# Kernel optimization log

Measured on AMD Instinct MI355X. Metric: run time of the kernel, lower is better.

Reference implementation:

```python
import jax, jax.numpy as jnp
import numpy as np

D_MODEL = 1024
N_HEADS = 16
HEAD_DIM = D_MODEL // N_HEADS
D_FF = 4096
LN_EPS = 1e-5


def setup_inputs() -> dict:
    key = jax.random.key(0)
    ks = jax.random.split(key, 13)
    s = lambda fan_in: 1.0 / np.sqrt(fan_in)
    return {
        "x": jax.random.normal(ks[0], (2, 2048, D_MODEL), dtype=jnp.float32),
        "w_qkv": jax.random.uniform(ks[1], (D_MODEL, 3 * D_MODEL), jnp.float32, -s(D_MODEL), s(D_MODEL)),
        "b_qkv": jax.random.uniform(ks[2], (3 * D_MODEL,), jnp.float32, -s(D_MODEL), s(D_MODEL)),
        "w_out": jax.random.uniform(ks[3], (D_MODEL, D_MODEL), jnp.float32, -s(D_MODEL), s(D_MODEL)),
        "b_out": jax.random.uniform(ks[4], (D_MODEL,), jnp.float32, -s(D_MODEL), s(D_MODEL)),
        "w_ff1": jax.random.uniform(ks[5], (D_MODEL, D_FF), jnp.float32, -s(D_MODEL), s(D_MODEL)),
        "b_ff1": jax.random.uniform(ks[6], (D_FF,), jnp.float32, -s(D_MODEL), s(D_MODEL)),
        "w_ff2": jax.random.uniform(ks[7], (D_FF, D_MODEL), jnp.float32, -s(D_FF), s(D_FF)),
        "b_ff2": jax.random.uniform(ks[8], (D_MODEL,), jnp.float32, -s(D_FF), s(D_FF)),
        "ln1_g": jnp.ones((D_MODEL,), jnp.float32),
        "ln1_b": jnp.zeros((D_MODEL,), jnp.float32),
        "ln2_g": jnp.ones((D_MODEL,), jnp.float32),
        "ln2_b": jnp.zeros((D_MODEL,), jnp.float32),
    }


def _layer_norm(x, g, b):
    mu = jnp.mean(x, axis=-1, keepdims=True)
    var = jnp.mean(jnp.square(x - mu), axis=-1, keepdims=True)
    return (x - mu) * jax.lax.rsqrt(var + LN_EPS) * g + b


def reference(x, w_qkv, b_qkv, w_out, b_out, w_ff1, b_ff1, w_ff2, b_ff2,
              ln1_g, ln1_b, ln2_g, ln2_b):
    B, S, D = x.shape
    scale = HEAD_DIM ** -0.5
    qkv = x @ w_qkv + b_qkv                                   # [B,S,3D]
    qkv = qkv.reshape(B, S, 3, N_HEADS, HEAD_DIM)
    q, k, v = (qkv[:, :, 0], qkv[:, :, 1], qkv[:, :, 2])      # [B,S,H,Dh]
    attn = jnp.einsum("bqhd,bkhd->bhqk", q, k) * scale        # [B,H,S,S]
    attn = jax.nn.softmax(attn, axis=-1)
    o = jnp.einsum("bhqk,bkhd->bqhd", attn, v).reshape(B, S, D)
    o = o @ w_out + b_out
    x = _layer_norm(x + o, ln1_g, ln1_b)
    # FFN: Linear -> exact GELU -> Linear (dropout = 0)
    h = jax.nn.gelu(x @ w_ff1 + b_ff1, approximate=False)
    ff = h @ w_ff2 + b_ff2
    x = _layer_norm(x + ff, ln2_g, ln2_b)
    return x
```

## Files before the change

kernel.cpp:

```cpp
#include <hip/hip_runtime.h>
#include <hip/hip_bf16.h>
#include <cstdint>
#include <cstddef>

using bf16 = __hip_bfloat16;
typedef __attribute__((ext_vector_type(8))) short bf16x8;
typedef __attribute__((ext_vector_type(4))) float f32x4;

#define TOKENS 4096
#define DMODEL 1024
#define DFF    4096
#define SEQ    2048
#define NHEAD  16
#define HDIM   64
#define KVBLK  64
#define NT     (SEQ / KVBLK)
#define QSCALE 0.1803368801111f

__device__ __forceinline__ void async16(const void* g, void* l) {
  __builtin_amdgcn_global_load_lds(
      (const __attribute__((address_space(1))) void*)g,
      (__attribute__((address_space(3))) void*)l, 16, 0, 0);
}

__device__ __forceinline__ f32x4 mfma16(bf16x8 a, bf16x8 b, f32x4 c) {
  return __builtin_amdgcn_mfma_f32_16x16x32_bf16(a, b, c, 0, 0, 0);
}

__device__ __forceinline__ float exp2_fast(float x) {
  float r;
  asm("v_exp_f32 %0, %1" : "=v"(r) : "v"(x));
  return r;
}

__device__ __forceinline__ float gelu_fast(float x) {
  const float z = fabsf(x) * 0.70710678118f;
  const float t = __builtin_amdgcn_rcpf(1.f + 0.3275911f * z);
  float p = 1.061405429f;
  p = p * t - 1.453152027f;
  p = p * t + 1.421413741f;
  p = p * t - 0.284496736f;
  p = p * t + 0.254829592f;
  const float e = exp2_fast(-z * z * 1.44269504089f);
  float erf = 1.f - p * t * e;
  erf = (x < 0.f) ? -erf : erf;
  return 0.5f * x * (1.f + erf);
}

__global__ void cast_bf16_k(const float* __restrict__ src, bf16* __restrict__ dst, int n) {
  int i = (blockIdx.x * blockDim.x + threadIdx.x) * 4;
  if (i >= n) return;
  float4 v = *(const float4*)(src + i);
  dst[i + 0] = __float2bfloat16(v.x);
  dst[i + 1] = __float2bfloat16(v.y);
  dst[i + 2] = __float2bfloat16(v.z);
  dst[i + 3] = __float2bfloat16(v.w);
}

__global__ void transpose_cast_k(const float* __restrict__ src, bf16* __restrict__ dst,
                                 int K, int N) {
  __shared__ float tile[32][33];
  int nt = blockIdx.x * 32, kt = blockIdx.y * 32;
  int tx = threadIdx.x, ty = threadIdx.y;
  #pragma unroll
  for (int i = 0; i < 32; i += 8)
    tile[ty + i][tx] = src[(size_t)(kt + ty + i) * N + nt + tx];
  __syncthreads();
  #pragma unroll
  for (int i = 0; i < 32; i += 8)
    dst[(size_t)(nt + ty + i) * K + kt + tx] = __float2bfloat16(tile[tx][ty + i]);
}

template <int EPI, int BN>
__global__ __launch_bounds__(256, 2)
void gemm_bt(const bf16* __restrict__ A, const bf16* __restrict__ Bt,
             const float* __restrict__ bias, int M, int N, int K,
             float* __restrict__ outf, bf16* __restrict__ outb,
             const float* __restrict__ resid,
             bf16* __restrict__ Qb, bf16* __restrict__ Kb, bf16* __restrict__ Vtb) {
  constexpr int MR = (BN == 128) ? 4 : 2;
  __shared__ bf16 Al[2][128 * 32];
  __shared__ bf16 Bl[2][BN * 32];
  const int t = threadIdx.x;
  const int nwg = gridDim.x * gridDim.y;
  const int flat = blockIdx.y * gridDim.x + blockIdx.x;
  const int swz = (flat & 7) * (nwg >> 3) + (flat >> 3);
  const int bm = (swz / gridDim.x) * 128, bn = (swz % gridDim.x) * BN;
  const int wid = t >> 6, lane = t & 63, g = lane >> 4, r = lane & 15;
  const int wr = (BN == 128) ? (wid >> 1) * 64 : wid * 32;
  const int wc = (BN == 128) ? (wid & 1) * 64 : 0;

  const f32x4 zero = {0.f, 0.f, 0.f, 0.f};
  f32x4 acc[MR][4];
  #pragma unroll
  for (int i = 0; i < MR; i++)
    #pragma unroll
    for (int j = 0; j < 4; j++) acc[i][j] = zero;

  const int ar0 = t >> 2, ac = (t & 3) * 8;
  const int ar1 = ar0 + 64;
  const int ach0 = t * 16, ach1 = ach0 + 4096;

  const int NK = K >> 5;
  #define STAGE(ktile, pb)                                                          \
    do {                                                                            \
      const int kk = (ktile) << 5;                                                  \
      async16(A + (size_t)(bm + ar0) * K + kk + ac, (char*)Al[pb] + ach0);          \
      async16(A + (size_t)(bm + ar1) * K + kk + ac, (char*)Al[pb] + ach1);          \
      async16(Bt + (size_t)(bn + ar0) * K + kk + ac, (char*)Bl[pb] + ach0);         \
      if constexpr (BN == 128)                                                      \
        async16(Bt + (size_t)(bn + ar1) * K + kk + ac, (char*)Bl[pb] + ach1);       \
    } while (0)

  STAGE(0, 0);
  asm volatile("s_waitcnt vmcnt(0)" ::: "memory");
  __builtin_amdgcn_s_barrier();

  #pragma unroll 1
  for (int it = 0; it < NK; ++it) {
    const int cur = it & 1;
    if (it + 1 < NK) STAGE(it + 1, cur ^ 1);
    bf16x8 af[MR], bfr[4];
    #pragma unroll
    for (int mt = 0; mt < MR; mt++)
      af[mt] = *(const bf16x8*)&Al[cur][(wr + mt * 16 + r) * 32 + 8 * g];
    #pragma unroll
    for (int nt = 0; nt < 4; nt++)
      bfr[nt] = *(const bf16x8*)&Bl[cur][(wc + nt * 16 + r) * 32 + 8 * g];
    #pragma unroll
    for (int mt = 0; mt < MR; mt++)
      #pragma unroll
      for (int nt = 0; nt < 4; nt++)
        acc[mt][nt] = mfma16(af[mt], bfr[nt], acc[mt][nt]);
    __builtin_amdgcn_sched_barrier(0);
    asm volatile("s_waitcnt vmcnt(0)" ::: "memory");
    __builtin_amdgcn_s_barrier();
  }
  #undef STAGE

  #pragma unroll
  for (int nt = 0; nt < 4; nt++) {
    const int col = bn + wc + nt * 16 + r;
    const float bv = bias[col];
    #pragma unroll
    for (int mt = 0; mt < MR; mt++) {
      #pragma unroll
      for (int j = 0; j < 4; j++) {
        const int row = bm + wr + mt * 16 + 4 * g + j;
        float v = acc[mt][nt][j] + bv;
        if constexpr (EPI == 0) {
          const int part = col >> 10, hd = col & 1023, h = hd >> 6, d = hd & 63;
          const int b_ = row >> 11, s_ = row & 2047;
          if (part == 0) {
            Qb[((size_t)(b_ * NHEAD + h) * SEQ + s_) * HDIM + d] =
                __float2bfloat16(v * QSCALE);
          } else if (part == 1) {
            Kb[((size_t)(b_ * NHEAD + h) * SEQ + s_) * HDIM + d] = __float2bfloat16(v);
          } else {
            Vtb[((size_t)(b_ * NHEAD + h) * HDIM + d) * SEQ + s_] = __float2bfloat16(v);
          }
        } else if constexpr (EPI == 1) {
          const size_t idx = (size_t)row * N + col;
          outf[idx] = v + resid[idx];
        } else {
          const size_t idx = (size_t)row * N + col;
          outb[idx] = __float2bfloat16(gelu_fast(v));
        }
      }
    }
  }
}

__global__ __launch_bounds__(256, 4)
void attn_k(const bf16* __restrict__ Q, const bf16* __restrict__ Km,
            const bf16* __restrict__ Vt, bf16* __restrict__ O) {
  __shared__ bf16 Kl[2][KVBLK * 64];
  __shared__ bf16 Vl[2][KVBLK * 64];
  __shared__ bf16 P[4][16 * 64];
  const int b = blockIdx.x;
  const int bswz = (b & 7) * 128 + (b >> 3);
  const int bh = bswz >> 5, qb = bswz & 31;
  const int t = threadIdx.x, wid = t >> 6, lane = t & 63, g = lane >> 4, r = lane & 15;
  const int q0 = qb * 64 + wid * 16;
  const bf16* Qp = Q + (size_t)bh * SEQ * HDIM;
  const char* Kc = (const char*)(Km + (size_t)bh * SEQ * HDIM);
  const char* Vc = (const char*)(Vt + (size_t)bh * HDIM * SEQ);

  const bf16x8 qf0 = *(const bf16x8*)&Qp[(q0 + r) * HDIM + 8 * g];
  const bf16x8 qf1 = *(const bf16x8*)&Qp[(q0 + r) * HDIM + 8 * g + 32];

  const int o0 = wid * 2048 + lane * 16, o1 = o0 + 1024;
  const int cs0 = ((((o0 >> 4) & 7) ^ ((o0 >> 7) & 7)) << 4);
  const int cs1 = ((((o1 >> 4) & 7) ^ ((o1 >> 7) & 7)) << 4);
  const int kso0 = (o0 & ~127) + cs0, kso1 = (o1 & ~127) + cs1;
  const int vso0 = (o0 >> 7) * (SEQ * 2) + cs0, vso1 = (o1 >> 7) * (SEQ * 2) + cs1;

  const f32x4 zero = {0.f, 0.f, 0.f, 0.f};
  f32x4 oacc[4];
  #pragma unroll
  for (int i = 0; i < 4; i++) oacc[i] = zero;
  float mrow = -1e30f, lrow = 0.f;
  bf16* pl = P[wid];
  const int cA = ((g ^ (r & 7)) << 3), cB = (((g + 4) ^ (r & 7)) << 3);

  {
    char* kd = (char*)Kl[0]; char* vd = (char*)Vl[0];
    async16(Kc + kso0, kd + o0); async16(Kc + kso1, kd + o1);
    async16(Vc + vso0, vd + o0); async16(Vc + vso1, vd + o1);
  }

  #pragma unroll 1
  for (int tt = 0; tt < NT; ++tt) {
    if (tt + 1 < NT) {
      const char* ks = Kc + (tt + 1) * (KVBLK * HDIM * 2);
      const char* vs = Vc + (tt + 1) * (KVBLK * 2);
      char* kd = (char*)Kl[(tt + 1) & 1]; char* vd = (char*)Vl[(tt + 1) & 1];
      async16(ks + kso0, kd + o0); async16(ks + kso1, kd + o1);
      async16(vs + vso0, vd + o0); async16(vs + vso1, vd + o1);
      asm volatile("s_waitcnt vmcnt(4)" ::: "memory");
    } else {
      asm volatile("s_waitcnt vmcnt(0)" ::: "memory");
    }
    __builtin_amdgcn_sched_barrier(0);
    __builtin_amdgcn_s_barrier();
    __builtin_amdgcn_sched_barrier(0);

    const bf16* kbuf = Kl[tt & 1];
    const bf16* vbuf = Vl[tt & 1];

    f32x4 sacc[4];
    #pragma unroll
    for (int kt = 0; kt < 4; kt++) {
      const bf16* krow = kbuf + (kt * 16 + r) * 64;
      bf16x8 ka = *(const bf16x8*)&krow[cA];
      bf16x8 kb = *(const bf16x8*)&krow[cB];
      f32x4 s = zero;
      s = mfma16(ka, qf0, s);
      s = mfma16(kb, qf1, s);
      sacc[kt] = s;
    }

    float m0 = fmaxf(fmaxf(sacc[0][0], sacc[0][1]), fmaxf(sacc[0][2], sacc[0][3]));
    float m1 = fmaxf(fmaxf(sacc[1][0], sacc[1][1]), fmaxf(sacc[1][2], sacc[1][3]));
    float m2 = fmaxf(fmaxf(sacc[2][0], sacc[2][1]), fmaxf(sacc[2][2], sacc[2][3]));
    float m3 = fmaxf(fmaxf(sacc[3][0], sacc[3][1]), fmaxf(sacc[3][2], sacc[3][3]));
    float mx = fmaxf(fmaxf(m0, m1), fmaxf(m2, m3));
    mx = fmaxf(mx, __shfl_xor(mx, 16));
    mx = fmaxf(mx, __shfl_xor(mx, 32));
    const bool grow = !__all(mx <= mrow + 8.f);
    float corr = 1.f;
    if (grow) {
      const float mn = fmaxf(mrow, mx);
      corr = exp2_fast(mrow - mn);
      mrow = mn;
    }
    float sum = 0.f;
    float sv[4][4];
    #pragma unroll
    for (int kt = 0; kt < 4; kt++)
      #pragma unroll
      for (int j = 0; j < 4; j++) {
        const float p = exp2_fast(sacc[kt][j] - mrow);
        sv[kt][j] = p;
        sum += p;
      }
    sum += __shfl_xor(sum, 16);
    sum += __shfl_xor(sum, 32);
    lrow = lrow * corr + sum;

    #pragma unroll
    for (int kt = 0; kt < 4; kt++) {
      bf16 pk[4] = {__float2bfloat16(sv[kt][0]), __float2bfloat16(sv[kt][1]),
                    __float2bfloat16(sv[kt][2]), __float2bfloat16(sv[kt][3])};
      const int pc = (((kt * 2 + (g >> 1)) ^ (r & 7)) << 4) + ((g & 1) << 3);
      *(short4*)((char*)pl + r * 128 + pc) = *(const short4*)pk;
    }
    asm volatile("s_waitcnt lgkmcnt(0)" ::: "memory");
    __builtin_amdgcn_sched_barrier(0);
    const bf16x8 pf0 = *(const bf16x8*)((const char*)pl + r * 128 + (cA << 1));
    const bf16x8 pf1 = *(const bf16x8*)((const char*)pl + r * 128 + (cB << 1));

    if (grow) {
      float cq[4];
      #pragma unroll
      for (int j = 0; j < 4; j++) cq[j] = __shfl(corr, 4 * g + j);
      #pragma unroll
      for (int dt = 0; dt < 4; dt++)
        #pragma unroll
        for (int j = 0; j < 4; j++) oacc[dt][j] *= cq[j];
    }

    #pragma unroll
    for (int dt = 0; dt < 4; dt++) {
      const bf16* vrow = vbuf + (dt * 16 + r) * 64;
      bf16x8 v0 = *(const bf16x8*)&vrow[cA];
      bf16x8 v1 = *(const bf16x8*)&vrow[cB];
      oacc[dt] = mfma16(pf0, v0, oacc[dt]);
      oacc[dt] = mfma16(pf1, v1, oacc[dt]);
    }
    __builtin_amdgcn_sched_barrier(0);
    __builtin_amdgcn_s_barrier();
  }

  float lq[4];
  #pragma unroll
  for (int j = 0; j < 4; j++) lq[j] = __shfl(lrow, 4 * g + j);
  const int b_ = bh >> 4, h = bh & 15;
  #pragma unroll
  for (int dt = 0; dt < 4; dt++)
    #pragma unroll
    for (int j = 0; j < 4; j++) {
      const int tok = b_ * SEQ + q0 + 4 * g + j;
      O[(size_t)tok * DMODEL + h * HDIM + dt * 16 + r] =
          __float2bfloat16(oacc[dt][j] / lq[j]);
    }
}

__global__ __launch_bounds__(256)
void ln_k(const float* __restrict__ in, const float* __restrict__ gw,
          const float* __restrict__ bw, float* __restrict__ outf,
          bf16* __restrict__ outb) {
  const int row = blockIdx.x, t = threadIdx.x;
  const float4 v = *(const float4*)(in + (size_t)row * DMODEL + t * 4);
  float s = v.x + v.y + v.z + v.w;
  float s2 = v.x * v.x + v.y * v.y + v.z * v.z + v.w * v.w;
  #pragma unroll
  for (int m = 1; m < 64; m <<= 1) { s += __shfl_xor(s, m); s2 += __shfl_xor(s2, m); }
  __shared__ float red[8];
  const int wid = t >> 6, lane = t & 63;
  if (lane == 0) { red[wid] = s; red[4 + wid] = s2; }
  __syncthreads();
  s = red[0] + red[1] + red[2] + red[3];
  s2 = red[4] + red[5] + red[6] + red[7];
  const float mu = s * (1.f / DMODEL);
  const float rstd = rsqrtf(s2 * (1.f / DMODEL) - mu * mu + 1e-5f);
  const float4 gv = *(const float4*)(gw + t * 4);
  const float4 bv = *(const float4*)(bw + t * 4);
  float o0 = (v.x - mu) * rstd * gv.x + bv.x;
  float o1 = (v.y - mu) * rstd * gv.y + bv.y;
  float o2 = (v.z - mu) * rstd * gv.z + bv.z;
  float o3 = (v.w - mu) * rstd * gv.w + bv.w;
  if (outf) {
    float4 ov = {o0, o1, o2, o3};
    *(float4*)(outf + (size_t)row * DMODEL + t * 4) = ov;
  }
  if (outb) {
    bf16* p = outb + (size_t)row * DMODEL + t * 4;
    p[0] = __float2bfloat16(o0); p[1] = __float2bfloat16(o1);
    p[2] = __float2bfloat16(o2); p[3] = __float2bfloat16(o3);
  }
}

extern "C" void kernel_launch(void* const* d_in, const int* in_sizes, int n_in,
                              void* d_out, int out_size, void* d_ws, size_t ws_size,
                              hipStream_t stream) {
  const float* x     = (const float*)d_in[0];
  const float* w_qkv = (const float*)d_in[1];
  const float* b_qkv = (const float*)d_in[2];
  const float* w_out = (const float*)d_in[3];
  const float* b_out = (const float*)d_in[4];
  const float* w_ff1 = (const float*)d_in[5];
  const float* b_ff1 = (const float*)d_in[6];
  const float* w_ff2 = (const float*)d_in[7];
  const float* b_ff2 = (const float*)d_in[8];
  const float* ln1_g = (const float*)d_in[9];
  const float* ln1_b = (const float*)d_in[10];
  const float* ln2_g = (const float*)d_in[11];
  const float* ln2_b = (const float*)d_in[12];
  float* out = (float*)d_out;

  char* base = (char*)d_ws;
  bf16* wqkvT = (bf16*)(base);
  bf16* woutT = (bf16*)(base + 6291456);
  bf16* wff1T = (bf16*)(base + 8388608);
  bf16* wff2T = (bf16*)(base + 16777216);
  bf16* Qb    = (bf16*)(base + 25165824);
  bf16* Kb    = (bf16*)(base + 33554432);
  bf16* Vtb   = (bf16*)(base + 41943040);
  bf16* xob   = (bf16*)(base + 50331648);
  bf16* hb    = (bf16*)(base + 25165824);
  float* y    = (float*)(base + 58720256);
  float* x1f  = (float*)(base + 75497472);
  bf16* x1b   = (bf16*)(base + 92274688);
  (void)in_sizes; (void)n_in; (void)out_size; (void)ws_size;

  dim3 tb(32, 8);
  transpose_cast_k<<<dim3(3072 / 32, 1024 / 32), tb, 0, stream>>>(w_qkv, wqkvT, 1024, 3072);
  transpose_cast_k<<<dim3(1024 / 32, 1024 / 32), tb, 0, stream>>>(w_out, woutT, 1024, 1024);
  transpose_cast_k<<<dim3(4096 / 32, 1024 / 32), tb, 0, stream>>>(w_ff1, wff1T, 1024, 4096);
  transpose_cast_k<<<dim3(1024 / 32, 4096 / 32), tb, 0, stream>>>(w_ff2, wff2T, 4096, 1024);
  cast_bf16_k<<<(TOKENS * DMODEL / 4 + 255) / 256, 256, 0, stream>>>(x, xob, TOKENS * DMODEL);

  gemm_bt<0, 128><<<dim3(3072 / 128, TOKENS / 128), 256, 0, stream>>>(
      xob, wqkvT, b_qkv, TOKENS, 3072, 1024, nullptr, nullptr, nullptr, Qb, Kb, Vtb);
  attn_k<<<dim3(1024), 256, 0, stream>>>(Qb, Kb, Vtb, xob);
  gemm_bt<1, 64><<<dim3(1024 / 64, TOKENS / 128), 256, 0, stream>>>(
      xob, woutT, b_out, TOKENS, 1024, 1024, y, nullptr, x, nullptr, nullptr, nullptr);
  ln_k<<<TOKENS, 256, 0, stream>>>(y, ln1_g, ln1_b, x1f, x1b);
  gemm_bt<2, 128><<<dim3(4096 / 128, TOKENS / 128), 256, 0, stream>>>(
      x1b, wff1T, b_ff1, TOKENS, 4096, 1024, nullptr, hb, nullptr, nullptr, nullptr, nullptr);
  gemm_bt<1, 64><<<dim3(1024 / 64, TOKENS / 128), 256, 0, stream>>>(
      hb, wff2T, b_ff2, TOKENS, 1024, 4096, y, nullptr, x1f, nullptr, nullptr, nullptr);
  ln_k<<<TOKENS, 256, 0, stream>>>(y, ln2_g, ln2_b, out, nullptr);
}
```

Baseline: 279.4 us.

## Split-K the two N=1024 GEMMs and fuse partial sum, bias, residual into LayerNorm

The out-projection and FF2 GEMMs are launched with a z-dimension of 2, each half of K writing a raw fp32 partial to a separate workspace buffer. The LayerNorm kernel now sums both partials with the bias and residual before normalizing. This doubles the block count for the under-filled N=1024 GEMMs to improve CU occupancy. The cost is an extra fp32 partial write and read per token row, and reuse of workspace regions for dead buffers.

Measured after the change: 270.2 us. 3.3% less time.

```diff
diff --git a/kernel.cpp b/kernel.cpp
--- a/kernel.cpp
+++ b/kernel.cpp
@@ -75,8 +75,8 @@
 __global__ __launch_bounds__(256, 2)
 void gemm_bt(const bf16* __restrict__ A, const bf16* __restrict__ Bt,
              const float* __restrict__ bias, int M, int N, int K,
-             float* __restrict__ outf, bf16* __restrict__ outb,
-             const float* __restrict__ resid,
+             float* __restrict__ outf, float* __restrict__ outf2,
+             bf16* __restrict__ outb,
              bf16* __restrict__ Qb, bf16* __restrict__ Kb, bf16* __restrict__ Vtb) {
   constexpr int MR = (BN == 128) ? 4 : 2;
   __shared__ bf16 Al[2][128 * 32];
@@ -86,6 +86,9 @@
   const int flat = blockIdx.y * gridDim.x + blockIdx.x;
   const int swz = (flat & 7) * (nwg >> 3) + (flat >> 3);
   const int bm = (swz / gridDim.x) * 128, bn = (swz % gridDim.x) * BN;
+  const int kz = blockIdx.z;
+  const int Ksub = K / gridDim.z;
+  const int kb0 = kz * Ksub;
   const int wid = t >> 6, lane = t & 63, g = lane >> 4, r = lane & 15;
   const int wr = (BN == 128) ? (wid >> 1) * 64 : wid * 32;
   const int wc = (BN == 128) ? (wid & 1) * 64 : 0;
@@ -101,10 +104,10 @@
   const int ar1 = ar0 + 64;
   const int ach0 = t * 16, ach1 = ach0 + 4096;
 
-  const int NK = K >> 5;
+  const int NK = Ksub >> 5;
   #define STAGE(ktile, pb)                                                          \
     do {                                                                            \
-      const int kk = (ktile) << 5;                                                  \
+      const int kk = kb0 + ((ktile) << 5);                                          \
       async16(A + (size_t)(bm + ar0) * K + kk + ac, (char*)Al[pb] + ach0);          \
       async16(A + (size_t)(bm + ar1) * K + kk + ac, (char*)Al[pb] + ach1);          \
       async16(Bt + (size_t)(bn + ar0) * K + kk + ac, (char*)Bl[pb] + ach0);         \
@@ -138,10 +141,11 @@
   }
   #undef STAGE
 
+  float* __restrict__ pdst = kz ? outf2 : outf;
   #pragma unroll
   for (int nt = 0; nt < 4; nt++) {
     const int col = bn + wc + nt * 16 + r;
-    const float bv = bias[col];
+    const float bv = (EPI == 3) ? 0.f : bias[col];
     #pragma unroll
     for (int mt = 0; mt < MR; mt++) {
       #pragma unroll
@@ -159,12 +163,10 @@
           } else {
             Vtb[((size_t)(b_ * NHEAD + h) * HDIM + d) * SEQ + s_] = __float2bfloat16(v);
           }
-        } else if constexpr (EPI == 1) {
-          const size_t idx = (size_t)row * N + col;
-          outf[idx] = v + resid[idx];
+        } else if constexpr (EPI == 3) {
+          pdst[(size_t)row * N + col] = v;
         } else {
-          const size_t idx = (size_t)row * N + col;
-          outb[idx] = __float2bfloat16(gelu_fast(v));
+          outb[(size_t)row * N + col] = __float2bfloat16(gelu_fast(v));
         }
       }
     }
@@ -317,11 +319,21 @@
 }
 
 __global__ __launch_bounds__(256)
-void ln_k(const float* __restrict__ in, const float* __restrict__ gw,
-          const float* __restrict__ bw, float* __restrict__ outf,
-          bf16* __restrict__ outb) {
+void ln_fused_k(const float* __restrict__ p0, const float* __restrict__ p1,
+                const float* __restrict__ bias2, const float* __restrict__ resid,
+                const float* __restrict__ gw, const float* __restrict__ bw,
+                float* __restrict__ outf, bf16* __restrict__ outb) {
   const int row = blockIdx.x, t = threadIdx.x;
-  const float4 v = *(const float4*)(in + (size_t)row * DMODEL + t * 4);
+  const size_t base = (size_t)row * DMODEL + t * 4;
+  const float4 a = *(const float4*)(p0 + base);
+  const float4 b = *(const float4*)(p1 + base);
+  const float4 rr = *(const float4*)(resid + base);
+  const float4 bb = *(const float4*)(bias2 + t * 4);
+  float4 v;
+  v.x = a.x + b.x + rr.x + bb.x;
+  v.y = a.y + b.y + rr.y + bb.y;
+  v.z = a.z + b.z + rr.z + bb.z;
+  v.w = a.w + b.w + rr.w + bb.w;
   float s = v.x + v.y + v.z + v.w;
   float s2 = v.x * v.x + v.y * v.y + v.z * v.z + v.w * v.w;
   #pragma unroll
@@ -342,10 +354,10 @@
   float o3 = (v.w - mu) * rstd * gv.w + bv.w;
   if (outf) {
     float4 ov = {o0, o1, o2, o3};
-    *(float4*)(outf + (size_t)row * DMODEL + t * 4) = ov;
+    *(float4*)(outf + base) = ov;
   }
   if (outb) {
-    bf16* p = outb + (size_t)row * DMODEL + t * 4;
+    bf16* p = outb + base;
     p[0] = __float2bfloat16(o0); p[1] = __float2bfloat16(o1);
     p[2] = __float2bfloat16(o2); p[3] = __float2bfloat16(o3);
   }
@@ -379,7 +391,10 @@
   bf16* Vtb   = (bf16*)(base + 41943040);
   bf16* xob   = (bf16*)(base + 50331648);
   bf16* hb    = (bf16*)(base + 25165824);
-  float* y    = (float*)(base + 58720256);
+  float* pA0  = (float*)(base + 25165824);
+  float* pA1  = (float*)(base + 58720256);
+  float* pB0  = (float*)(base + 58720256);
+  float* pB1  = (float*)(base);
   float* x1f  = (float*)(base + 75497472);
   bf16* x1b   = (bf16*)(base + 92274688);
   (void)in_sizes; (void)n_in; (void)out_size; (void)ws_size;
@@ -394,12 +409,12 @@
   gemm_bt<0, 128><<<dim3(3072 / 128, TOKENS / 128), 256, 0, stream>>>(
       xob, wqkvT, b_qkv, TOKENS, 3072, 1024, nullptr, nullptr, nullptr, Qb, Kb, Vtb);
   attn_k<<<dim3(1024), 256, 0, stream>>>(Qb, Kb, Vtb, xob);
-  gemm_bt<1, 64><<<dim3(1024 / 64, TOKENS / 128), 256, 0, stream>>>(
-      xob, woutT, b_out, TOKENS, 1024, 1024, y, nullptr, x, nullptr, nullptr, nullptr);
-  ln_k<<<TOKENS, 256, 0, stream>>>(y, ln1_g, ln1_b, x1f, x1b);
+  gemm_bt<3, 64><<<dim3(1024 / 64, TOKENS / 128, 2), 256, 0, stream>>>(
+      xob, woutT, b_out, TOKENS, 1024, 1024, pA0, pA1, nullptr, nullptr, nullptr, nullptr);
+  ln_fused_k<<<TOKENS, 256, 0, stream>>>(pA0, pA1, b_out, x, ln1_g, ln1_b, x1f, x1b);
   gemm_bt<2, 128><<<dim3(4096 / 128, TOKENS / 128), 256, 0, stream>>>(
-      x1b, wff1T, b_ff1, TOKENS, 4096, 1024, nullptr, hb, nullptr, nullptr, nullptr, nullptr);
-  gemm_bt<1, 64><<<dim3(1024 / 64, TOKENS / 128), 256, 0, stream>>>(
-      hb, wff2T, b_ff2, TOKENS, 1024, 4096, y, nullptr, x1f, nullptr, nullptr, nullptr);
-  ln_k<<<TOKENS, 256, 0, stream>>>(y, ln2_g, ln2_b, out, nullptr);
-}
+      x1b, wff1T, b_ff1, TOKENS, 4096, 1024, nullptr, nullptr, hb, nullptr, nullptr, nullptr);
+  gemm_bt<3, 64><<<dim3(1024 / 64, TOKENS / 128, 2), 256, 0, stream>>>(
+      hb, wff2T, b_ff2, TOKENS, 1024, 4096, pB0, pB1, nullptr, nullptr, nullptr, nullptr);
+  ln_fused_k<<<TOKENS, 256, 0, stream>>>(pB0, pB1, b_ff2, x1f, ln2_g, ln2_b, out, nullptr);
+}
```
